# Kernel tuning notes

Measured on AMD Instinct MI355X. Metric: run time of the kernel, lower is better.

Reference implementation:

```python
import jax, jax.numpy as jnp
import numpy as np

B, T, I, H, O, L = 64, 2048, 128, 256, 1, 2


def _lstm_layer(x, w_ih, w_hh, b_ih, b_hh):
    # x: [B, T, in]; w_ih: [4H, in]; w_hh: [4H, H]; biases: [4H]
    # Batch the input-side GEMM across all timesteps (torch gate order: i, f, g, o)
    xg = jnp.einsum('bti,gi->btg', x, w_ih) + b_ih + b_hh  # [B, T, 4H]
    h0 = jnp.zeros((x.shape[0], w_hh.shape[1]), x.dtype)
    c0 = jnp.zeros_like(h0)

    def step(carry, xt):
        h, c = carry
        g = xt + h @ w_hh.T  # [B, 4H]
        i, f, gg, o = jnp.split(g, 4, axis=-1)
        i = jax.nn.sigmoid(i)
        f = jax.nn.sigmoid(f)
        gg = jnp.tanh(gg)
        o = jax.nn.sigmoid(o)
        c = f * c + i * gg
        h = o * jnp.tanh(c)
        return (h, c), h

    _, hs = jax.lax.scan(step, (h0, c0), jnp.swapaxes(xg, 0, 1))  # [T, B, H]
    return jnp.swapaxes(hs, 0, 1)  # [B, T, H]


def setup_inputs() -> dict:
    key = jax.random.key(0)
    ks = jax.random.split(key, 11)
    s_i = 1.0 / np.sqrt(H)
    return {
        'x': jax.random.normal(ks[0], (B, T, I), jnp.float32),
        'w_ih0': jax.random.uniform(ks[1], (4 * H, I), jnp.float32, -s_i, s_i),
        'w_hh0': jax.random.uniform(ks[2], (4 * H, H), jnp.float32, -s_i, s_i),
        'b_ih0': jax.random.uniform(ks[3], (4 * H,), jnp.float32, -s_i, s_i),
        'b_hh0': jax.random.uniform(ks[4], (4 * H,), jnp.float32, -s_i, s_i),
        'w_ih1': jax.random.uniform(ks[5], (4 * H, H), jnp.float32, -s_i, s_i),
        'w_hh1': jax.random.uniform(ks[6], (4 * H, H), jnp.float32, -s_i, s_i),
        'b_ih1': jax.random.uniform(ks[7], (4 * H,), jnp.float32, -s_i, s_i),
        'b_hh1': jax.random.uniform(ks[8], (4 * H,), jnp.float32, -s_i, s_i),
        'fc_w': jax.random.uniform(ks[9], (O, H), jnp.float32, -s_i, s_i),
        'fc_b': jax.random.uniform(ks[10], (O,), jnp.float32, -s_i, s_i),
    }


def reference(x, w_ih0, w_hh0, b_ih0, b_hh0, w_ih1, w_hh1, b_ih1, b_hh1, fc_w, fc_b):
    h = _lstm_layer(x, w_ih0, w_hh0, b_ih0, b_hh0)
    h = _lstm_layer(h, w_ih1, w_hh1, b_ih1, b_hh1)
    h = jax.nn.relu(h)            # relu on full sequence output (as in source)
    last = h[:, -1, :]            # [B, H]
    return last @ fc_w.T + fc_b   # [B, O]
```

## Files before the change

kernel.cpp:

```cpp
#include <hip/hip_runtime.h>

#define NT 2048
#define NI 128
#define NH 256
#define WPG 32
#define BPG 8

typedef unsigned long long u64;

__device__ __forceinline__ float sigm(float v) {
  return 1.0f / (1.0f + __expf(-v));
}
__device__ __forceinline__ float tanh_fast(float v) {
  v = fminf(fmaxf(v, -15.0f), 15.0f);
  float e = __expf(-2.0f * v);
  return (1.0f - e) / (1.0f + e);
}

__device__ __forceinline__ int ld_flag(const int* p) {
  return __hip_atomic_load(p, __ATOMIC_RELAXED, __HIP_MEMORY_SCOPE_AGENT);
}
__device__ __forceinline__ void st_flag(int* p, int v) {
  __hip_atomic_store(p, v, __ATOMIC_RELAXED, __HIP_MEMORY_SCOPE_AGENT);
}
__device__ __forceinline__ void st_h(float* p, float v) {
  __hip_atomic_store(p, v, __ATOMIC_RELAXED, __HIP_MEMORY_SCOPE_AGENT);
}
__device__ __forceinline__ u64 ld_h64(const u64* p) {
  return __hip_atomic_load(p, __ATOMIC_RELAXED, __HIP_MEMORY_SCOPE_AGENT);
}

__global__ __launch_bounds__(512, 2) void lstm_persistent(
    const float* __restrict__ x,
    const float* __restrict__ wih0, const float* __restrict__ whh0,
    const float* __restrict__ bih0, const float* __restrict__ bhh0,
    const float* __restrict__ wih1, const float* __restrict__ whh1,
    const float* __restrict__ bih1, const float* __restrict__ bhh1,
    const float* __restrict__ fcw, const float* __restrict__ fcb,
    float* __restrict__ out,
    float* __restrict__ h0buf, float* __restrict__ h1buf,
    int* __restrict__ flags)
{
  extern __shared__ float sm[];
  float* zz   = sm;
  float* pL0  = zz + 4 * 640;
  float* pL1  = pL0 + 1024;
  float* bias = pL1 + 1024;

  const int tid = threadIdx.x;
  const int bid = blockIdx.x;
  const int g = bid & 7;
  const int j = bid >> 3;
  const int b0 = g * BPG;
  int* fA = flags + g * WPG;
  int* fB = flags + 256 + g * WPG;

  const bool isL0 = (tid < 256);
  const int lt = tid & 255;
  const int r = lt & 31;
  const int s = lt >> 5;
  const int gate = r >> 3;
  const int R = gate * NH + j * 8 + (r & 7);

  float wreg[64];
  if (isL0) {
    const int kbase = s * 48;
#pragma unroll
    for (int kk = 0; kk < 48; ++kk) {
      int k = kbase + kk;
      wreg[kk] = (k < NI) ? wih0[R * NI + k] : whh0[R * NH + (k - NI)];
    }
#pragma unroll
    for (int kk = 48; kk < 64; ++kk) wreg[kk] = 0.0f;
  } else {
    const int kbase = s * 64;
#pragma unroll
    for (int kk = 0; kk < 64; ++kk) {
      int k = kbase + kk;
      wreg[kk] = (k < NH) ? wih1[R * NH + k] : whh1[R * NH + (k - NH)];
    }
  }
  if (tid < 32) bias[tid] = bih0[R] + bhh0[R];
  if (tid >= 256 && tid < 288) bias[32 + r] = bih1[R] + bhh1[R];

  float cellA = 0.0f, cellB = 0.0f;
  u64 rh0 = 0, rh1 = 0;
  float4 xv = make_float4(0.f, 0.f, 0.f, 0.f);
  if (tid < 128) {
    const int b = tid >> 5, i4 = (tid & 31) * 4;
    xv = *reinterpret_cast<const float4*>(
        x + ((size_t)(b0 + b) * NT + 0) * NI + i4);
  }
  __syncthreads();

  for (int it = 0; it <= NT; ++it) {
#pragma unroll 1
    for (int half = 0; half < 2; ++half) {
      const int xb = half ? 4 : 0;
      int* fSelf  = half ? fB : fA;
      int* fOther = half ? fA : fB;
      const int nit = half ? (it + 1) : it;
      const int oxb = half ? 0 : 4;

      if (tid < 256) {
        if (tid < 128 && it < NT) {
          const int b = tid >> 5, i4 = (tid & 31) * 4;
          *reinterpret_cast<float4*>(&zz[b * 640 + i4]) = xv;
        }
        {
          const int m0 = tid, m1 = 256 + tid;
          *reinterpret_cast<u64*>(&zz[(m0 >> 7) * 640 + 128 + (m0 & 127) * 2]) = rh0;
          *reinterpret_cast<u64*>(&zz[(m1 >> 7) * 640 + 128 + (m1 & 127) * 2]) = rh1;
        }
      } else {
        const int p = tid - 256;
        const int m0 = p, m1 = 256 + p;
        *reinterpret_cast<u64*>(&zz[(m0 >> 7) * 640 + 384 + (m0 & 127) * 2]) = rh0;
        *reinterpret_cast<u64*>(&zz[(m1 >> 7) * 640 + 384 + (m1 & 127) * 2]) = rh1;
      }
      __syncthreads();

      if (isL0) {
        if (it < NT) {
          float acc0 = 0.f, acc1 = 0.f, acc2 = 0.f, acc3 = 0.f;
          const int kb = s * 48;
#pragma unroll
          for (int c = 0; c < 12; ++c) {
            const float4 h0v = *reinterpret_cast<const float4*>(&zz[0 * 640 + kb + c * 4]);
            const float4 h1v = *reinterpret_cast<const float4*>(&zz[1 * 640 + kb + c * 4]);
            const float4 h2v = *reinterpret_cast<const float4*>(&zz[2 * 640 + kb + c * 4]);
            const float4 h3v = *reinterpret_cast<const float4*>(&zz[3 * 640 + kb + c * 4]);
            const float w0 = wreg[c * 4 + 0], w1 = wreg[c * 4 + 1];
            const float w2 = wreg[c * 4 + 2], w3 = wreg[c * 4 + 3];
            acc0 = fmaf(w0, h0v.x, fmaf(w1, h0v.y, fmaf(w2, h0v.z, fmaf(w3, h0v.w, acc0))));
            acc1 = fmaf(w0, h1v.x, fmaf(w1, h1v.y, fmaf(w2, h1v.z, fmaf(w3, h1v.w, acc1))));
            acc2 = fmaf(w0, h2v.x, fmaf(w1, h2v.y, fmaf(w2, h2v.z, fmaf(w3, h2v.w, acc2))));
            acc3 = fmaf(w0, h3v.x, fmaf(w1, h3v.y, fmaf(w2, h3v.z, fmaf(w3, h3v.w, acc3))));
          }
          pL0[s * 128 + 0 * 32 + r] = acc0;
          pL0[s * 128 + 1 * 32 + r] = acc1;
          pL0[s * 128 + 2 * 32 + r] = acc2;
          pL0[s * 128 + 3 * 32 + r] = acc3;
        }
      } else if (it >= 1) {
        float acc0 = 0.f, acc1 = 0.f, acc2 = 0.f, acc3 = 0.f;
        const int kb = s * 64;
#pragma unroll
        for (int c = 0; c < 16; ++c) {
          const float4 h0v = *reinterpret_cast<const float4*>(&zz[0 * 640 + 128 + kb + c * 4]);
          const float4 h1v = *reinterpret_cast<const float4*>(&zz[1 * 640 + 128 + kb + c * 4]);
          const float4 h2v = *reinterpret_cast<const float4*>(&zz[2 * 640 + 128 + kb + c * 4]);
          const float4 h3v = *reinterpret_cast<const float4*>(&zz[3 * 640 + 128 + kb + c * 4]);
          const float w0 = wreg[c * 4 + 0], w1 = wreg[c * 4 + 1];
          const float w2 = wreg[c * 4 + 2], w3 = wreg[c * 4 + 3];
          acc0 = fmaf(w0, h0v.x, fmaf(w1, h0v.y, fmaf(w2, h0v.z, fmaf(w3, h0v.w, acc0))));
          acc1 = fmaf(w0, h1v.x, fmaf(w1, h1v.y, fmaf(w2, h1v.z, fmaf(w3, h1v.w, acc1))));
          acc2 = fmaf(w0, h2v.x, fmaf(w1, h2v.y, fmaf(w2, h2v.z, fmaf(w3, h2v.w, acc2))));
          acc3 = fmaf(w0, h3v.x, fmaf(w1, h3v.y, fmaf(w2, h3v.z, fmaf(w3, h3v.w, acc3))));
        }
        pL1[s * 128 + 0 * 32 + r] = acc0;
        pL1[s * 128 + 1 * 32 + r] = acc1;
        pL1[s * 128 + 2 * 32 + r] = acc2;
        pL1[s * 128 + 3 * 32 + r] = acc3;
      }

      if (tid < WPG) {
        int guard = 0;
        while (ld_flag(&fOther[tid]) < nit) {
          __builtin_amdgcn_s_sleep(1);
          if (++guard > 100000000) break;
        }
      }
      __syncthreads();

      if (nit <= NT) {
        const int p0 = (nit - 1) & 1;
        const int p1 = nit & 1;
        if (tid < 256) {
          const int m0 = tid, m1 = 256 + tid;
          rh0 = ld_h64(reinterpret_cast<const u64*>(
              h0buf + ((size_t)p0 * 64 + (b0 + oxb + (m0 >> 7))) * NH + (m0 & 127) * 2));
          rh1 = ld_h64(reinterpret_cast<const u64*>(
              h0buf + ((size_t)p0 * 64 + (b0 + oxb + (m1 >> 7))) * NH + (m1 & 127) * 2));
          if (tid < 128 && nit < NT) {
            const int b = tid >> 5, i4 = (tid & 31) * 4;
            xv = *reinterpret_cast<const float4*>(
                x + ((size_t)(b0 + oxb + b) * NT + (size_t)nit) * NI + i4);
          }
        } else {
          const int p = tid - 256;
          const int m0 = p, m1 = 256 + p;
          rh0 = ld_h64(reinterpret_cast<const u64*>(
              h1buf + ((size_t)p1 * 64 + (b0 + oxb + (m0 >> 7))) * NH + (m0 & 127) * 2));
          rh1 = ld_h64(reinterpret_cast<const u64*>(
              h1buf + ((size_t)p1 * 64 + (b0 + oxb + (m1 >> 7))) * NH + (m1 & 127) * 2));
        }
      }

      if (tid < 128) {
        if (it < NT) {
          const int b = tid >> 5;
          float sum = bias[r];
#pragma unroll
          for (int s2 = 0; s2 < 8; ++s2) sum += pL0[s2 * 128 + b * 32 + r];
          const float v8  = __shfl_xor(sum, 8);
          const float v16 = __shfl_xor(sum, 16);
          const float v24 = __shfl_xor(v8, 16);
          float q0 = sum, q1 = v8, q2 = v16, q3 = v24, tq;
          if (gate & 1) { tq = q0; q0 = q1; q1 = tq; tq = q2; q2 = q3; q3 = tq; }
          if (gate & 2) { tq = q0; q0 = q2; q2 = tq; tq = q1; q1 = q3; q3 = tq; }
          const float ii = sigm(q0), ff = sigm(q1), gt = tanh_fast(q2), oo = sigm(q3);
          float c = (half ? cellB : cellA);
          c = ff * c + ii * gt;
          if (half) cellB = c; else cellA = c;
          const float h = oo * tanh_fast(c);
          if (r < 8)
            st_h(&h0buf[((size_t)(it & 1) * 64 + (b0 + xb + b)) * NH + j * 8 + r], h);
        }
      } else if (tid >= 256 && tid < 384 && it >= 1) {
        const int b = (tid - 256) >> 5;
        float sum = bias[32 + r];
#pragma unroll
        for (int s2 = 0; s2 < 8; ++s2) sum += pL1[s2 * 128 + b * 32 + r];
        const float v8  = __shfl_xor(sum, 8);
        const float v16 = __shfl_xor(sum, 16);
        const float v24 = __shfl_xor(v8, 16);
        float q0 = sum, q1 = v8, q2 = v16, q3 = v24, tq;
        if (gate & 1) { tq = q0; q0 = q1; q1 = tq; tq = q2; q2 = q3; q3 = tq; }
        if (gate & 2) { tq = q0; q0 = q2; q2 = tq; tq = q1; q1 = q3; q3 = tq; }
        const float ii = sigm(q0), ff = sigm(q1), gt = tanh_fast(q2), oo = sigm(q3);
        float c = (half ? cellB : cellA);
        c = ff * c + ii * gt;
        if (half) cellB = c; else cellA = c;
        const float h = oo * tanh_fast(c);
        if (r < 8)
          st_h(&h1buf[((size_t)((it - 1) & 1) * 64 + (b0 + xb + b)) * NH + j * 8 + r], h);
      }
      asm volatile("s_waitcnt vmcnt(0)" ::: "memory");
      __syncthreads();
      if (tid == 0) st_flag(&fSelf[j], it + 1);
    }
  }

  if (j == 0) {
    if (tid < WPG) {
      int guard = 0;
      while (ld_flag(&fA[tid]) < NT + 1 || ld_flag(&fB[tid]) < NT + 1) {
        __builtin_amdgcn_s_sleep(1);
        if (++guard > 100000000) break;
      }
    }
    __syncthreads();
    const int bb = tid >> 6, lane = tid & 63;
    const float* hrow = h1buf + ((size_t)(((NT - 1) & 1)) * 64 + (b0 + bb)) * NH;
    const u64 u0 = ld_h64(reinterpret_cast<const u64*>(hrow + lane * 4));
    const u64 u1 = ld_h64(reinterpret_cast<const u64*>(hrow + lane * 4 + 2));
    const float ha = __uint_as_float((unsigned)u0);
    const float hb = __uint_as_float((unsigned)(u0 >> 32));
    const float hc = __uint_as_float((unsigned)u1);
    const float hd = __uint_as_float((unsigned)(u1 >> 32));
    const float4 w4 = *reinterpret_cast<const float4*>(fcw + lane * 4);
    float p = fmaxf(ha, 0.f) * w4.x + fmaxf(hb, 0.f) * w4.y +
              fmaxf(hc, 0.f) * w4.z + fmaxf(hd, 0.f) * w4.w;
#pragma unroll
    for (int off = 32; off >= 1; off >>= 1) p += __shfl_down(p, off, 64);
    if (lane == 0) out[b0 + bb] = p + fcb[0];
  }
}

extern "C" void kernel_launch(void* const* d_in, const int* in_sizes, int n_in,
                              void* d_out, int out_size, void* d_ws, size_t ws_size,
                              hipStream_t stream) {
  (void)in_sizes; (void)n_in; (void)out_size; (void)ws_size;
  const float* x    = (const float*)d_in[0];
  const float* wih0 = (const float*)d_in[1];
  const float* whh0 = (const float*)d_in[2];
  const float* bih0 = (const float*)d_in[3];
  const float* bhh0 = (const float*)d_in[4];
  const float* wih1 = (const float*)d_in[5];
  const float* whh1 = (const float*)d_in[6];
  const float* bih1 = (const float*)d_in[7];
  const float* bhh1 = (const float*)d_in[8];
  const float* fcw  = (const float*)d_in[9];
  const float* fcb  = (const float*)d_in[10];
  float* out = (float*)d_out;

  float* ws = (float*)d_ws;
  float* h0buf = ws;
  float* h1buf = ws + 2 * 64 * 256;
  int* flags = (int*)(ws + 4 * 64 * 256);

  const size_t zbytes = (size_t)(4 * 64 * 256) * sizeof(float) + 512 * sizeof(int);
  hipMemsetAsync(d_ws, 0, zbytes, stream);

  size_t shmem = 96 * 1024;
  if (hipFuncSetAttribute(reinterpret_cast<const void*>(lstm_persistent),
                          hipFuncAttributeMaxDynamicSharedMemorySize,
                          (int)shmem) != hipSuccess) {
    shmem = 4672 * sizeof(float);
  }

  hipLaunchKernelGGL(lstm_persistent, dim3(256), dim3(512), shmem, stream,
                     x, wih0, whh0, bih0, bhh0, wih1, whh1, bih1, bhh1,
                     fcw, fcb, out, h0buf, h1buf, flags);
}
```

Baseline: 10.15 ms.

## Give each thread all four gates and reduce partial sums with DPP

```diff
diff --git a/kernel.cpp b/kernel.cpp
--- a/kernel.cpp
+++ b/kernel.cpp
@@ -16,6 +16,12 @@
   float e = __expf(-2.0f * v);
   return (1.0f - e) / (1.0f + e);
 }
+__device__ __forceinline__ float lstm_act(float gi, float gf, float gg, float go,
+                                          float& c) {
+  const float ii = sigm(gi), ff = sigm(gf), gt = tanh_fast(gg), oo = sigm(go);
+  c = ff * c + ii * gt;
+  return oo * tanh_fast(c);
+}
 
 __device__ __forceinline__ int ld_flag(const int* p) {
   return __hip_atomic_load(p, __ATOMIC_RELAXED, __HIP_MEMORY_SCOPE_AGENT);
@@ -30,7 +36,20 @@
   return __hip_atomic_load(p, __ATOMIC_RELAXED, __HIP_MEMORY_SCOPE_AGENT);
 }
 
-__global__ __launch_bounds__(512, 2) void lstm_persistent(
+template <int CTRL>
+__device__ __forceinline__ float dppadd(float x) {
+  int s = __builtin_amdgcn_update_dpp(0, __float_as_int(x), CTRL, 0xf, 0xf, true);
+  return x + __int_as_float(s);
+}
+__device__ __forceinline__ float red16(float v) {
+  v = dppadd<0xB1>(v);
+  v = dppadd<0x4E>(v);
+  v = dppadd<0x141>(v);
+  v = dppadd<0x140>(v);
+  return v;
+}
+
+__global__ __launch_bounds__(512, 1) void lstm_persistent(
     const float* __restrict__ x,
     const float* __restrict__ wih0, const float* __restrict__ whh0,
     const float* __restrict__ bih0, const float* __restrict__ bhh0,
@@ -42,10 +61,7 @@
     int* __restrict__ flags)
 {
   extern __shared__ float sm[];
-  float* zz   = sm;
-  float* pL0  = zz + 4 * 640;
-  float* pL1  = pL0 + 1024;
-  float* bias = pL1 + 1024;
+  float* zz = sm;
 
   const int tid = threadIdx.x;
   const int bid = blockIdx.x;
@@ -56,112 +72,149 @@
   int* fB = flags + 256 + g * WPG;
 
   const bool isL0 = (tid < 256);
-  const int lt = tid & 255;
-  const int r = lt & 31;
-  const int s = lt >> 5;
-  const int gate = r >> 3;
-  const int R = gate * NH + j * 8 + (r & 7);
-
-  float wreg[64];
+  const int lane = tid & 63;
+  const int wv = (tid & 255) >> 6;
+  const int ks = lane & 15;
+  const int rg2 = (lane >> 4) & 1;
+  const int bg = lane >> 5;
+  const int u = wv * 2 + rg2;
+  const int col = j * 8 + u;
+
+  float w[4][32];
+  float bs[4];
   if (isL0) {
-    const int kbase = s * 48;
-#pragma unroll
-    for (int kk = 0; kk < 48; ++kk) {
-      int k = kbase + kk;
-      wreg[kk] = (k < NI) ? wih0[R * NI + k] : whh0[R * NH + (k - NI)];
+#pragma unroll
+    for (int gt = 0; gt < 4; ++gt) {
+      const int R = gt * NH + col;
+      bs[gt] = bih0[R] + bhh0[R];
+#pragma unroll
+      for (int c = 0; c < 6; ++c)
+#pragma unroll
+        for (int e = 0; e < 4; ++e) {
+          const int k = ks * 4 + 64 * c + e;
+          w[gt][c * 4 + e] = (k < NI) ? wih0[R * NI + k] : whh0[R * NH + (k - NI)];
+        }
     }
-#pragma unroll
-    for (int kk = 48; kk < 64; ++kk) wreg[kk] = 0.0f;
   } else {
-    const int kbase = s * 64;
-#pragma unroll
-    for (int kk = 0; kk < 64; ++kk) {
-      int k = kbase + kk;
-      wreg[kk] = (k < NH) ? wih1[R * NH + k] : whh1[R * NH + (k - NH)];
+#pragma unroll
+    for (int gt = 0; gt < 4; ++gt) {
+      const int R = gt * NH + col;
+      bs[gt] = bih1[R] + bhh1[R];
+#pragma unroll
+      for (int c = 0; c < 8; ++c)
+#pragma unroll
+        for (int e = 0; e < 4; ++e) {
+          const int k = ks * 4 + 64 * c + e;
+          w[gt][c * 4 + e] = (k < NH) ? wih1[R * NH + k] : whh1[R * NH + (k - NH)];
+        }
     }
   }
-  if (tid < 32) bias[tid] = bih0[R] + bhh0[R];
-  if (tid >= 256 && tid < 288) bias[32 + r] = bih1[R] + bhh1[R];
-
-  float cellA = 0.0f, cellB = 0.0f;
+
+  float cellA0 = 0.f, cellA1 = 0.f, cellB0 = 0.f, cellB1 = 0.f;
   u64 rh0 = 0, rh1 = 0;
   float4 xv = make_float4(0.f, 0.f, 0.f, 0.f);
   if (tid < 128) {
-    const int b = tid >> 5, i4 = (tid & 31) * 4;
     xv = *reinterpret_cast<const float4*>(
-        x + ((size_t)(b0 + b) * NT + 0) * NI + i4);
+        x + (size_t)(b0 + (tid >> 5)) * NT * NI + (tid & 31) * 4);
   }
   __syncthreads();
 
+#pragma unroll 1
   for (int it = 0; it <= NT; ++it) {
-#pragma unroll 1
+#pragma unroll
     for (int half = 0; half < 2; ++half) {
       const int xb = half ? 4 : 0;
-      int* fSelf  = half ? fB : fA;
+      int* fSelf = half ? fB : fA;
       int* fOther = half ? fA : fB;
-      const int nit = half ? (it + 1) : it;
+      const int nit = half ? it + 1 : it;
       const int oxb = half ? 0 : 4;
 
-      if (tid < 256) {
-        if (tid < 128 && it < NT) {
-          const int b = tid >> 5, i4 = (tid & 31) * 4;
-          *reinterpret_cast<float4*>(&zz[b * 640 + i4]) = xv;
-        }
-        {
-          const int m0 = tid, m1 = 256 + tid;
-          *reinterpret_cast<u64*>(&zz[(m0 >> 7) * 640 + 128 + (m0 & 127) * 2]) = rh0;
-          *reinterpret_cast<u64*>(&zz[(m1 >> 7) * 640 + 128 + (m1 & 127) * 2]) = rh1;
-        }
-      } else {
-        const int p = tid - 256;
-        const int m0 = p, m1 = 256 + p;
-        *reinterpret_cast<u64*>(&zz[(m0 >> 7) * 640 + 384 + (m0 & 127) * 2]) = rh0;
-        *reinterpret_cast<u64*>(&zz[(m1 >> 7) * 640 + 384 + (m1 & 127) * 2]) = rh1;
-      }
+      if (tid < 128 && it < NT)
+        *reinterpret_cast<float4*>(&zz[(tid >> 5) * 640 + (tid & 31) * 4]) = xv;
+      *reinterpret_cast<u64*>(&zz[(tid >> 7) * 640 + 128 + (tid & 127) * 2]) = rh0;
+      *reinterpret_cast<u64*>(&zz[(tid >> 7) * 640 + 384 + (tid & 127) * 2]) = rh1;
       __syncthreads();
 
       if (isL0) {
         if (it < NT) {
-          float acc0 = 0.f, acc1 = 0.f, acc2 = 0.f, acc3 = 0.f;
-          const int kb = s * 48;
-#pragma unroll
-          for (int c = 0; c < 12; ++c) {
-            const float4 h0v = *reinterpret_cast<const float4*>(&zz[0 * 640 + kb + c * 4]);
-            const float4 h1v = *reinterpret_cast<const float4*>(&zz[1 * 640 + kb + c * 4]);
-            const float4 h2v = *reinterpret_cast<const float4*>(&zz[2 * 640 + kb + c * 4]);
-            const float4 h3v = *reinterpret_cast<const float4*>(&zz[3 * 640 + kb + c * 4]);
-            const float w0 = wreg[c * 4 + 0], w1 = wreg[c * 4 + 1];
-            const float w2 = wreg[c * 4 + 2], w3 = wreg[c * 4 + 3];
-            acc0 = fmaf(w0, h0v.x, fmaf(w1, h0v.y, fmaf(w2, h0v.z, fmaf(w3, h0v.w, acc0))));
-            acc1 = fmaf(w0, h1v.x, fmaf(w1, h1v.y, fmaf(w2, h1v.z, fmaf(w3, h1v.w, acc1))));
-            acc2 = fmaf(w0, h2v.x, fmaf(w1, h2v.y, fmaf(w2, h2v.z, fmaf(w3, h2v.w, acc2))));
-            acc3 = fmaf(w0, h3v.x, fmaf(w1, h3v.y, fmaf(w2, h3v.z, fmaf(w3, h3v.w, acc3))));
-          }
-          pL0[s * 128 + 0 * 32 + r] = acc0;
-          pL0[s * 128 + 1 * 32 + r] = acc1;
-          pL0[s * 128 + 2 * 32 + r] = acc2;
-          pL0[s * 128 + 3 * 32 + r] = acc3;
-        }
-      } else if (it >= 1) {
-        float acc0 = 0.f, acc1 = 0.f, acc2 = 0.f, acc3 = 0.f;
-        const int kb = s * 64;
-#pragma unroll
-        for (int c = 0; c < 16; ++c) {
-          const float4 h0v = *reinterpret_cast<const float4*>(&zz[0 * 640 + 128 + kb + c * 4]);
-          const float4 h1v = *reinterpret_cast<const float4*>(&zz[1 * 640 + 128 + kb + c * 4]);
-          const float4 h2v = *reinterpret_cast<const float4*>(&zz[2 * 640 + 128 + kb + c * 4]);
-          const float4 h3v = *reinterpret_cast<const float4*>(&zz[3 * 640 + 128 + kb + c * 4]);
-          const float w0 = wreg[c * 4 + 0], w1 = wreg[c * 4 + 1];
-          const float w2 = wreg[c * 4 + 2], w3 = wreg[c * 4 + 3];
-          acc0 = fmaf(w0, h0v.x, fmaf(w1, h0v.y, fmaf(w2, h0v.z, fmaf(w3, h0v.w, acc0))));
-          acc1 = fmaf(w0, h1v.x, fmaf(w1, h1v.y, fmaf(w2, h1v.z, fmaf(w3, h1v.w, acc1))));
-          acc2 = fmaf(w0, h2v.x, fmaf(w1, h2v.y, fmaf(w2, h2v.z, fmaf(w3, h2v.w, acc2))));
-          acc3 = fmaf(w0, h3v.x, fmaf(w1, h3v.y, fmaf(w2, h3v.z, fmaf(w3, h3v.w, acc3))));
-        }
-        pL1[s * 128 + 0 * 32 + r] = acc0;
-        pL1[s * 128 + 1 * 32 + r] = acc1;
-        pL1[s * 128 + 2 * 32 + r] = acc2;
-        pL1[s * 128 + 3 * 32 + r] = acc3;
+          float acc[4][2] = {{0.f, 0.f}, {0.f, 0.f}, {0.f, 0.f}, {0.f, 0.f}};
+          const float* z0 = &zz[(bg * 2 + 0) * 640 + ks * 4];
+          const float* z1 = &zz[(bg * 2 + 1) * 640 + ks * 4];
+#pragma unroll
+          for (int c = 0; c < 6; ++c) {
+            const float4 v0 = *reinterpret_cast<const float4*>(z0 + 64 * c);
+            const float4 v1 = *reinterpret_cast<const float4*>(z1 + 64 * c);
+#pragma unroll
+            for (int gt = 0; gt < 4; ++gt) {
+              acc[gt][0] = fmaf(w[gt][c * 4 + 0], v0.x, acc[gt][0]);
+              acc[gt][0] = fmaf(w[gt][c * 4 + 1], v0.y, acc[gt][0]);
+              acc[gt][0] = fmaf(w[gt][c * 4 + 2], v0.z, acc[gt][0]);
+              acc[gt][0] = fmaf(w[gt][c * 4 + 3], v0.w, acc[gt][0]);
+              acc[gt][1] = fmaf(w[gt][c * 4 + 0], v1.x, acc[gt][1]);
+              acc[gt][1] = fmaf(w[gt][c * 4 + 1], v1.y, acc[gt][1]);
+              acc[gt][1] = fmaf(w[gt][c * 4 + 2], v1.z, acc[gt][1]);
+              acc[gt][1] = fmaf(w[gt][c * 4 + 3], v1.w, acc[gt][1]);
+            }
+          }
+#pragma unroll
+          for (int gt = 0; gt < 4; ++gt) {
+            acc[gt][0] = red16(acc[gt][0]);
+            acc[gt][1] = red16(acc[gt][1]);
+          }
+          float ca = half ? cellB0 : cellA0;
+          const float ha = lstm_act(acc[0][0] + bs[0], acc[1][0] + bs[1],
+                                    acc[2][0] + bs[2], acc[3][0] + bs[3], ca);
+          if (half) cellB0 = ca; else cellA0 = ca;
+          float cb = half ? cellB1 : cellA1;
+          const float hb = lstm_act(acc[0][1] + bs[0], acc[1][1] + bs[1],
+                                    acc[2][1] + bs[2], acc[3][1] + bs[3], cb);
+          if (half) cellB1 = cb; else cellA1 = cb;
+          if ((lane & 15) == 0) {
+            const size_t base = (size_t)(it & 1) * 64;
+            st_h(&h0buf[(base + (b0 + xb + bg * 2 + 0)) * NH + col], ha);
+            st_h(&h0buf[(base + (b0 + xb + bg * 2 + 1)) * NH + col], hb);
+          }
+        }
+      } else {
+        if (it >= 1) {
+          float acc[4][2] = {{0.f, 0.f}, {0.f, 0.f}, {0.f, 0.f}, {0.f, 0.f}};
+          const float* z0 = &zz[(bg * 2 + 0) * 640 + 128 + ks * 4];
+          const float* z1 = &zz[(bg * 2 + 1) * 640 + 128 + ks * 4];
+#pragma unroll
+          for (int c = 0; c < 8; ++c) {
+            const float4 v0 = *reinterpret_cast<const float4*>(z0 + 64 * c);
+            const float4 v1 = *reinterpret_cast<const float4*>(z1 + 64 * c);
+#pragma unroll
+            for (int gt = 0; gt < 4; ++gt) {
+              acc[gt][0] = fmaf(w[gt][c * 4 + 0], v0.x, acc[gt][0]);
+              acc[gt][0] = fmaf(w[gt][c * 4 + 1], v0.y, acc[gt][0]);
+              acc[gt][0] = fmaf(w[gt][c * 4 + 2], v0.z, acc[gt][0]);
+              acc[gt][0] = fmaf(w[gt][c * 4 + 3], v0.w, acc[gt][0]);
+              acc[gt][1] = fmaf(w[gt][c * 4 + 0], v1.x, acc[gt][1]);
+              acc[gt][1] = fmaf(w[gt][c * 4 + 1], v1.y, acc[gt][1]);
+              acc[gt][1] = fmaf(w[gt][c * 4 + 2], v1.z, acc[gt][1]);
+              acc[gt][1] = fmaf(w[gt][c * 4 + 3], v1.w, acc[gt][1]);
+            }
+          }
+#pragma unroll
+          for (int gt = 0; gt < 4; ++gt) {
+            acc[gt][0] = red16(acc[gt][0]);
+            acc[gt][1] = red16(acc[gt][1]);
+          }
+          float ca = half ? cellB0 : cellA0;
+          const float ha = lstm_act(acc[0][0] + bs[0], acc[1][0] + bs[1],
+                                    acc[2][0] + bs[2], acc[3][0] + bs[3], ca);
+          if (half) cellB0 = ca; else cellA0 = ca;
+          float cb = half ? cellB1 : cellA1;
+          const float hb = lstm_act(acc[0][1] + bs[0], acc[1][1] + bs[1],
+                                    acc[2][1] + bs[2], acc[3][1] + bs[3], cb);
+          if (half) cellB1 = cb; else cellA1 = cb;
+          if ((lane & 15) == 0) {
+            const size_t base = (size_t)((it - 1) & 1) * 64;
+            st_h(&h1buf[(base + (b0 + xb + bg * 2 + 0)) * NH + col], ha);
+            st_h(&h1buf[(base + (b0 + xb + bg * 2 + 1)) * NH + col], hb);
+          }
+        }
       }
 
       if (tid < WPG) {
@@ -176,68 +229,27 @@
       if (nit <= NT) {
         const int p0 = (nit - 1) & 1;
         const int p1 = nit & 1;
-        if (tid < 256) {
-          const int m0 = tid, m1 = 256 + tid;
-          rh0 = ld_h64(reinterpret_cast<const u64*>(
-              h0buf + ((size_t)p0 * 64 + (b0 + oxb + (m0 >> 7))) * NH + (m0 & 127) * 2));
-          rh1 = ld_h64(reinterpret_cast<const u64*>(
-              h0buf + ((size_t)p0 * 64 + (b0 + oxb + (m1 >> 7))) * NH + (m1 & 127) * 2));
-          if (tid < 128 && nit < NT) {
-            const int b = tid >> 5, i4 = (tid & 31) * 4;
-            xv = *reinterpret_cast<const float4*>(
-                x + ((size_t)(b0 + oxb + b) * NT + (size_t)nit) * NI + i4);
-          }
-        } else {
-          const int p = tid - 256;
-          const int m0 = p, m1 = 256 + p;
-          rh0 = ld_h64(reinterpret_cast<const u64*>(
-              h1buf + ((size_t)p1 * 64 + (b0 + oxb + (m0 >> 7))) * NH + (m0 & 127) * 2));
-          rh1 = ld_h64(reinterpret_cast<const u64*>(
-              h1buf + ((size_t)p1 * 64 + (b0 + oxb + (m1 >> 7))) * NH + (m1 & 127) * 2));
-        }
-      }
-
-      if (tid < 128) {
-        if (it < NT) {
-          const int b = tid >> 5;
-          float sum = bias[r];
-#pragma unroll
-          for (int s2 = 0; s2 < 8; ++s2) sum += pL0[s2 * 128 + b * 32 + r];
-          const float v8  = __shfl_xor(sum, 8);
-          const float v16 = __shfl_xor(sum, 16);
-          const float v24 = __shfl_xor(v8, 16);
-          float q0 = sum, q1 = v8, q2 = v16, q3 = v24, tq;
-          if (gate & 1) { tq = q0; q0 = q1; q1 = tq; tq = q2; q2 = q3; q3 = tq; }
-          if (gate & 2) { tq = q0; q0 = q2; q2 = tq; tq = q1; q1 = q3; q3 = tq; }
-          const float ii = sigm(q0), ff = sigm(q1), gt = tanh_fast(q2), oo = sigm(q3);
-          float c = (half ? cellB : cellA);
-          c = ff * c + ii * gt;
-          if (half) cellB = c; else cellA = c;
-          const float h = oo * tanh_fast(c);
-          if (r < 8)
-            st_h(&h0buf[((size_t)(it & 1) * 64 + (b0 + xb + b)) * NH + j * 8 + r], h);
-        }
-      } else if (tid >= 256 && tid < 384 && it >= 1) {
-        const int b = (tid - 256) >> 5;
-        float sum = bias[32 + r];
-#pragma unroll
-        for (int s2 = 0; s2 < 8; ++s2) sum += pL1[s2 * 128 + b * 32 + r];
-        const float v8  = __shfl_xor(sum, 8);
-        const float v16 = __shfl_xor(sum, 16);
-        const float v24 = __shfl_xor(v8, 16);
-        float q0 = sum, q1 = v8, q2 = v16, q3 = v24, tq;
-        if (gate & 1) { tq = q0; q0 = q1; q1 = tq; tq = q2; q2 = q3; q3 = tq; }
-        if (gate & 2) { tq = q0; q0 = q2; q2 = tq; tq = q1; q1 = q3; q3 = tq; }
-        const float ii = sigm(q0), ff = sigm(q1), gt = tanh_fast(q2), oo = sigm(q3);
-        float c = (half ? cellB : cellA);
-        c = ff * c + ii * gt;
-        if (half) cellB = c; else cellA = c;
-        const float h = oo * tanh_fast(c);
-        if (r < 8)
-          st_h(&h1buf[((size_t)((it - 1) & 1) * 64 + (b0 + xb + b)) * NH + j * 8 + r], h);
-      }
-      asm volatile("s_waitcnt vmcnt(0)" ::: "memory");
-      __syncthreads();
+        const int bl = tid >> 7, off = (tid & 127) * 2;
+        rh0 = ld_h64(reinterpret_cast<const u64*>(
+            h0buf + ((size_t)p0 * 64 + (b0 + oxb + bl)) * NH + off));
+        rh1 = ld_h64(reinterpret_cast<const u64*>(
+            h1buf + ((size_t)p1 * 64 + (b0 + oxb + bl)) * NH + off));
+        if (tid < 128 && nit < NT) {
+          xv = *reinterpret_cast<const float4*>(
+              x + ((size_t)(b0 + oxb + (tid >> 5)) * NT + (size_t)nit) * NI +
+              (tid & 31) * 4);
+        }
+      }
+
+      if (nit <= NT) {
+        if (tid < 128 && nit < NT)
+          asm volatile("s_waitcnt vmcnt(3)" ::: "memory");
+        else
+          asm volatile("s_waitcnt vmcnt(2)" ::: "memory");
+      } else {
+        asm volatile("s_waitcnt vmcnt(0)" ::: "memory");
+      }
+      __builtin_amdgcn_s_barrier();
       if (tid == 0) st_flag(&fSelf[j], it + 1);
     }
   }
@@ -251,20 +263,20 @@
       }
     }
     __syncthreads();
-    const int bb = tid >> 6, lane = tid & 63;
+    const int bb = tid >> 6, ln = tid & 63;
     const float* hrow = h1buf + ((size_t)(((NT - 1) & 1)) * 64 + (b0 + bb)) * NH;
-    const u64 u0 = ld_h64(reinterpret_cast<const u64*>(hrow + lane * 4));
-    const u64 u1 = ld_h64(reinterpret_cast<const u64*>(hrow + lane * 4 + 2));
+    const u64 u0 = ld_h64(reinterpret_cast<const u64*>(hrow + ln * 4));
+    const u64 u1 = ld_h64(reinterpret_cast<const u64*>(hrow + ln * 4 + 2));
     const float ha = __uint_as_float((unsigned)u0);
     const float hb = __uint_as_float((unsigned)(u0 >> 32));
     const float hc = __uint_as_float((unsigned)u1);
     const float hd = __uint_as_float((unsigned)(u1 >> 32));
-    const float4 w4 = *reinterpret_cast<const float4*>(fcw + lane * 4);
+    const float4 w4 = *reinterpret_cast<const float4*>(fcw + ln * 4);
     float p = fmaxf(ha, 0.f) * w4.x + fmaxf(hb, 0.f) * w4.y +
               fmaxf(hc, 0.f) * w4.z + fmaxf(hd, 0.f) * w4.w;
 #pragma unroll
     for (int off = 32; off >= 1; off >>= 1) p += __shfl_down(p, off, 64);
-    if (lane == 0) out[b0 + bb] = p + fcb[0];
+    if (ln == 0) out[b0 + bb] = p + fcb[0];
   }
 }
 
@@ -297,7 +309,7 @@
   if (hipFuncSetAttribute(reinterpret_cast<const void*>(lstm_persistent),
                           hipFuncAttributeMaxDynamicSharedMemorySize,
                           (int)shmem) != hipSuccess) {
-    shmem = 4672 * sizeof(float);
+    shmem = 2560 * sizeof(float);
   }
 
   hipLaunchKernelGGL(lstm_persistent, dim3(256), dim3(512), shmem, stream,
```

Measured after the change: 10.74 ms. +5.8%, slower.
